# Kernel tuning notes

Measured on AMD Instinct MI355X. Metric: run time of the kernel, lower is better.

Reference implementation:

```python
import jax, jax.numpy as jnp
import numpy as np

INPUT_DIM = 64
AUG_DIM = 64
STATE = INPUT_DIM + AUG_DIM  # 128
HIDDEN = 1024
T = 32
B, S = 64, 64


def setup_inputs() -> dict:
    key = jax.random.key(0)
    ks = jax.random.split(key, 12)

    def lin(kw, kb, out_d, in_d):
        scale = 1.0 / np.sqrt(in_d)
        W = jax.random.uniform(kw, (out_d, in_d), jnp.float32, -scale, scale)
        b = jax.random.uniform(kb, (out_d,), jnp.float32, -scale, scale)
        return W, b

    y0 = jax.random.normal(ks[0], (B, S, INPUT_DIM), jnp.float32)
    t = jnp.linspace(0.0, 1.0, T, dtype=jnp.float32)
    W_aug, b_aug = lin(ks[1], ks[2], AUG_DIM, INPUT_DIM)
    W0, b0 = lin(ks[3], ks[4], HIDDEN, STATE)
    W1, b1 = lin(ks[5], ks[6], HIDDEN, HIDDEN)
    W2, b2 = lin(ks[7], ks[8], HIDDEN, HIDDEN)
    W3, b3 = lin(ks[9], ks[10], STATE, HIDDEN)
    return {"y0": y0, "t": t, "W_aug": W_aug, "b_aug": b_aug,
            "W0": W0, "b0": b0, "W1": W1, "b1": b1,
            "W2": W2, "b2": b2, "W3": W3, "b3": b3}


def reference(y0, t, W_aug, b_aug, W0, b0, W1, b1, W2, b2, W3, b3):
    # augment: y0 [B,S,Din] -> [B,S,Din+Daug]
    y_aug = jnp.einsum('bsd,ad->bsa', y0, W_aug) + b_aug
    y = jnp.concatenate([y0, y_aug], axis=-1)  # [B,S,STATE]

    dt = t[1] - t[0]

    def mlp(z):
        h = jnp.tanh(jnp.einsum('bsd,hd->bsh', z, W0) + b0)
        h = jnp.tanh(jnp.einsum('bsh,gh->bsg', h, W1) + b1)
        h = jnp.tanh(jnp.einsum('bsh,gh->bsg', h, W2) + b2)
        return jnp.einsum('bsh,dh->bsd', h, W3) + b3

    def step(y_cur, _):
        y_next = y_cur + mlp(y_cur) * dt
        return y_next, None

    # forward only uses the final state: out[:, -1, :, :input_dim]
    y_final, _ = jax.lax.scan(step, y, None, length=T - 1)
    return y_final[..., :INPUT_DIM]
```

## Files before the change

### kernel.cpp

```cpp
#include <hip/hip_runtime.h>

typedef _Float16 h8 __attribute__((ext_vector_type(8)));
typedef float f32x4 __attribute__((ext_vector_type(4)));
typedef int  i4 __attribute__((ext_vector_type(4)));

#define NTHREADS 1024
#define ROWS 16
#define NBLK 256

#define SMEM_BYTES 163840

#define GLOAD16(gp, lp) __builtin_amdgcn_global_load_lds( \
    (const __attribute__((address_space(1))) void*)(gp),  \
    (__attribute__((address_space(3))) void*)(lp), 16, 0, 0)

__device__ __forceinline__ float fast_tanh(float x) {
    float e = __expf(2.0f * x);
    return 1.0f - 2.0f / (e + 1.0f);
}

__device__ __forceinline__ void lightbar() {
    asm volatile("s_waitcnt lgkmcnt(0)" ::: "memory");
    __builtin_amdgcn_sched_barrier(0);
    __builtin_amdgcn_s_barrier();
    __builtin_amdgcn_sched_barrier(0);
}

template<int K>
__global__ void __launch_bounds__(256) pack_kernel(const float* __restrict__ src,
                                                   _Float16* __restrict__ dst, int nfrag) {
    constexpr int NK = K / 32;
    int idx = blockIdx.x * 256 + threadIdx.x;
    if (idx >= nfrag) return;
    int lane = idx & 63;
    int ct   = (idx >> 6) & 3;
    int kk   = (idx >> 8) % NK;
    int w    = idx / (256 * NK);
    int col  = w * 64 + ct * 16 + (lane & 15);
    int kb   = kk * 32 + (lane >> 4) * 8;
    const float* s = src + (size_t)col * K + kb;
    f32x4 v0 = *(const f32x4*)s;
    f32x4 v1 = *(const f32x4*)(s + 4);
    h8 h;
    h[0]=(_Float16)v0[0]; h[1]=(_Float16)v0[1]; h[2]=(_Float16)v0[2]; h[3]=(_Float16)v0[3];
    h[4]=(_Float16)v1[0]; h[5]=(_Float16)v1[1]; h[6]=(_Float16)v1[2]; h[7]=(_Float16)v1[3];
    *(h8*)(dst + (size_t)idx * 8) = h;
}

__global__ void __launch_bounds__(256) pack8_kernel(const float* __restrict__ src,
                                                    char* __restrict__ dst, int nfrag) {
    int idx = blockIdx.x * 256 + threadIdx.x;
    if (idx >= nfrag) return;
    int lane = idx & 63;
    int ct   = (idx >> 6) & 3;
    int kk   = (idx >> 8) & 15;
    int w    = idx >> 12;
    int col  = w * 64 + ct * 16 + (lane & 15);
    int kb   = kk * 64 + (lane >> 4) * 16;
    const float* s = src + (size_t)col * 1024 + kb;
    union { char q[16]; i4 v; } u;
#pragma unroll
    for (int j = 0; j < 16; ++j)
        u.q[j] = (char)__float2int_rn(s[j] * 4064.0f);
    *(i4*)(dst + (size_t)idx * 16) = u.v;
}

__global__ void __launch_bounds__(256) pack3q_kernel(const float* __restrict__ src,
                                                     char* __restrict__ dst, int nfrag) {
    int idx = blockIdx.x * 256 + threadIdx.x;
    if (idx >= nfrag) return;
    int lane = idx & 63;
    int kk   = (idx >> 6) & 15;
    int cg   = idx >> 10;
    int col  = cg * 16 + (lane & 15);
    int kb   = kk * 64 + (lane >> 4) * 16;
    const float* s = src + (size_t)col * 1024 + kb;
    union { char q[16]; i4 v; } u;
#pragma unroll
    for (int j = 0; j < 16; ++j)
        u.q[j] = (char)__float2int_rn(s[j] * 4064.0f);
    *(i4*)(dst + (size_t)idx * 16) = u.v;
}

__device__ __forceinline__ void mlp0(const char* __restrict__ src, char* __restrict__ dst,
                                     const _Float16* __restrict__ Wp, f32x4 bv,
                                     int w, int l15, int lhi, int lane)
{
    constexpr int NK = 4;
    const int colbase = w * 64;
    const _Float16* wb = Wp + (size_t)w * NK * 2048 + lane * 8;

    f32x4 acc[4];
#pragma unroll
    for (int ct = 0; ct < 4; ++ct) {
        f32x4 a; a[0] = bv[ct]; a[1] = bv[ct]; a[2] = bv[ct]; a[3] = bv[ct];
        acc[ct] = a;
    }

    h8 bE[4], bO[4], aE, aO;
    auto loadB = [&](h8* b, int kk) {
#pragma unroll
        for (int ct = 0; ct < 4; ++ct)
            b[ct] = *(const h8*)(wb + (size_t)kk * 2048 + ct * 512);
    };
    auto loadA = [&](h8& a, int kk) {
        int byte = (l15 * 256 + kk * 64 + lhi * 16) ^ ((l15 & 7) << 4);
        a = *(const h8*)(src + byte);
    };
    auto mfma4 = [&](h8& a, h8* b) {
        __builtin_amdgcn_s_setprio(1);
#pragma unroll
        for (int ct = 0; ct < 4; ++ct)
            acc[ct] = __builtin_amdgcn_mfma_f32_16x16x32_f16(a, b[ct], acc[ct], 0, 0, 0);
        __builtin_amdgcn_s_setprio(0);
    };

    loadB(bE, 0); loadA(aE, 0);
    loadB(bO, 1); loadA(aO, 1);
    mfma4(aE, bE);
    loadB(bE, 2); loadA(aE, 2);
    mfma4(aO, bO);
    loadB(bO, 3); loadA(aO, 3);
    mfma4(aE, bE);
    mfma4(aO, bO);

#pragma unroll
    for (int ct = 0; ct < 4; ++ct)
#pragma unroll
        for (int j = 0; j < 4; ++j) {
            int row = lhi * 4 + j;
            int gc = colbase + ct * 16 + l15;
            int q = __float2int_rn(fast_tanh(acc[ct][j]) * 127.0f);
            int byte = (row * 1024 + gc) ^ ((row & 7) << 4);
            *(char*)(dst + byte) = (char)q;
        }
}

__device__ __forceinline__ void stage2(const char* wbl, char* ringW)
{
#pragma unroll
    for (int c = 0; c < 2; ++c) {
        const char* g = wbl + (size_t)c * 4096;
        char* l = ringW + c * 4096;
#pragma unroll
        for (int ct = 0; ct < 4; ++ct)
            GLOAD16(g + ct * 1024, l + ct * 1024);
    }
}

__device__ __forceinline__ void mlp8c(const char* __restrict__ src, char* __restrict__ dst,
                                      const char* wbl, char* ringW, const char* ringR,
                                      f32x4 bv, int w, int l15, int lhi,
                                      const char* nextwb)
{
    const int colbase = w * 64;
    i4 acc[4];
#pragma unroll
    for (int ct = 0; ct < 4; ++ct) { i4 z; z[0]=0; z[1]=0; z[2]=0; z[3]=0; acc[ct] = z; }

    i4 B0, B1, B2, B3, A;
    auto readSlot = [&](int kk) {
        const char* sl = ringR + (kk & 1) * 4096;
        B0 = *(const i4*)(sl);
        B1 = *(const i4*)(sl + 1024);
        B2 = *(const i4*)(sl + 2048);
        B3 = *(const i4*)(sl + 3072);
        int byte = (l15 * 1024 + kk * 64 + lhi * 16) ^ ((l15 & 7) << 4);
        A = *(const i4*)(src + byte);
    };
    auto mfma4 = [&]() {
        __builtin_amdgcn_s_setprio(1);
        acc[0] = __builtin_amdgcn_mfma_i32_16x16x64_i8(A, B0, acc[0], 0, 0, 0);
        acc[1] = __builtin_amdgcn_mfma_i32_16x16x64_i8(A, B1, acc[1], 0, 0, 0);
        acc[2] = __builtin_amdgcn_mfma_i32_16x16x64_i8(A, B2, acc[2], 0, 0, 0);
        acc[3] = __builtin_amdgcn_mfma_i32_16x16x64_i8(A, B3, acc[3], 0, 0, 0);
        __builtin_amdgcn_s_setprio(0);
    };

#pragma unroll 1
    for (int kk = 0; kk < 15; ++kk) {
        asm volatile("s_waitcnt vmcnt(4)" ::: "memory");
        __builtin_amdgcn_sched_barrier(0);
        readSlot(kk);
        asm volatile("s_waitcnt lgkmcnt(0)" ::: "memory");
        __builtin_amdgcn_sched_barrier(0);
        if (kk < 14) {
            const char* g = wbl + (size_t)(kk + 2) * 4096;
            char* l = ringW + (kk & 1) * 4096;
#pragma unroll
            for (int ct = 0; ct < 4; ++ct)
                GLOAD16(g + ct * 1024, l + ct * 1024);
        }
        __builtin_amdgcn_sched_barrier(0);
        mfma4();
    }
    asm volatile("s_waitcnt vmcnt(0)" ::: "memory");
    __builtin_amdgcn_sched_barrier(0);
    readSlot(15);
    asm volatile("s_waitcnt lgkmcnt(0)" ::: "memory");
    __builtin_amdgcn_sched_barrier(0);
    stage2(nextwb, ringW);
    __builtin_amdgcn_sched_barrier(0);
    mfma4();

    const float DEQ = 1.0f / 516128.0f;
#pragma unroll
    for (int ct = 0; ct < 4; ++ct) {
        int gc = colbase + ct * 16 + l15;
#pragma unroll
        for (int j = 0; j < 4; ++j) {
            int row = lhi * 4 + j;
            float v = fast_tanh((float)acc[ct][j] * DEQ + bv[ct]);
            int q = __float2int_rn(v * 127.0f);
            int byte = (row * 1024 + gc) ^ ((row & 7) << 4);
            *(char*)(dst + byte) = (char)q;
        }
    }
}

__global__ void
__attribute__((amdgpu_flat_work_group_size(NTHREADS, NTHREADS)))
node_kernel(const float* __restrict__ y0,
            const float* __restrict__ tarr,
            const float* __restrict__ W_aug,
            const float* __restrict__ b_aug,
            const float* __restrict__ b0,
            const float* __restrict__ b1,
            const float* __restrict__ b2,
            const float* __restrict__ b3,
            const _Float16* __restrict__ W0p,
            const char* __restrict__ W1q,
            const char* __restrict__ W2q,
            const char* __restrict__ W3q,
            float* __restrict__ out)
{
    __shared__ __align__(16) char smem[SMEM_BYTES];
    char* buf8A = smem;
    char* buf8B = smem + 16384;
    char* Yh    = smem + 16384;
    i4*   red   = (i4*)(smem + 24576);
    float* Yf   = (float*)smem;
    char* ring  = smem + 32768;

    const int tid  = threadIdx.x;
    const int lane = tid & 63;
    const int w    = tid >> 6;
    const int l15  = lane & 15;
    const int lhi  = lane >> 4;
    const int row0 = blockIdx.x * ROWS;

    const float dtv = tarr[1] - tarr[0];

    if (tid < 256) {
        int idx = tid * 4;
        int r = idx >> 6;
        int c = idx & 63;
        f32x4 v = *(const f32x4*)(y0 + (size_t)(row0 + r) * 64 + c);
        *(f32x4*)(Yf + r * 128 + c) = v;
    }
    __syncthreads();

    {
        int r = tid >> 6;
        int a0 = tid & 63;
        float acc = b_aug[a0];
        for (int d = 0; d < 64; ++d)
            acc += Yf[r * 128 + d] * W_aug[a0 * 64 + d];
        __syncthreads();
        Yf[r * 128 + 64 + a0] = acc;
    }
    __syncthreads();

    const int g = w * 16 + l15;
    f32x4 yreg;
    if (w < 8) {
#pragma unroll
        for (int j = 0; j < 4; ++j)
            yreg[j] = Yf[(lhi * 4 + j) * 128 + g];
    }
    h8 yh0;
    int yh0_byte;
    if (tid < 256) {
        int r = tid >> 4;
        int c = (tid & 15) * 8;
        const float* p = Yf + r * 128 + c;
#pragma unroll
        for (int j = 0; j < 8; ++j) yh0[j] = (_Float16)p[j];
        yh0_byte = ((r * 128 + c) * 2) ^ ((r & 7) << 4);
    }
    __syncthreads();
    if (tid < 256) *(h8*)(Yh + yh0_byte) = yh0;
    __syncthreads();

    const char* wb1 = W1q + (size_t)w * 65536 + lane * 16;
    const char* wb2 = W2q + (size_t)w * 65536 + lane * 16;
    char* ringW = ring + w * 8192;
    const char* ringR = ringW + lane * 16;

    f32x4 b0v, b1v, b2v;
#pragma unroll
    for (int ct = 0; ct < 4; ++ct) {
        b0v[ct] = b0[w * 64 + ct * 16 + l15];
        b1v[ct] = b1[w * 64 + ct * 16 + l15];
        b2v[ct] = b2[w * 64 + ct * 16 + l15];
    }
    const int cg  = w & 7;
    const int kk0 = (w >> 3) * 8;
    const char* wb3 = W3q + (size_t)cg * 16384 + lane * 16;
    const float b3v = (w < 8) ? b3[g] : 0.0f;
    const float DEQ3 = 1.0f / 516128.0f;

    stage2(wb1, ringW);

    for (int s = 0; s < 31; ++s) {
        mlp0(Yh, buf8A, W0p, b0v, w, l15, lhi, lane);
        lightbar();

        mlp8c(buf8A, buf8B, wb1, ringW, ringR, b1v, w, l15, lhi, wb2);
        lightbar();

        mlp8c(buf8B, buf8A, wb2, ringW, ringR, b2v, w, l15, lhi, wb1);
        lightbar();

        {
            i4 acc3; acc3[0]=0; acc3[1]=0; acc3[2]=0; acc3[3]=0;
            i4 c3E, c3O, x3E, x3O;
            auto loadB3 = [&](i4& b, int kk) {
                b = *(const i4*)(wb3 + (size_t)kk * 1024);
            };
            auto loadA3 = [&](i4& a, int kk) {
                int byte = (l15 * 1024 + kk * 64 + lhi * 16) ^ ((l15 & 7) << 4);
                a = *(const i4*)(buf8A + byte);
            };
            loadB3(c3E, kk0 + 0); loadA3(x3E, kk0 + 0);
#pragma unroll
            for (int q = 0; q < 3; ++q) {
                loadB3(c3O, kk0 + 2 * q + 1); loadA3(x3O, kk0 + 2 * q + 1);
                acc3 = __builtin_amdgcn_mfma_i32_16x16x64_i8(x3E, c3E, acc3, 0, 0, 0);
                loadB3(c3E, kk0 + 2 * q + 2); loadA3(x3E, kk0 + 2 * q + 2);
                acc3 = __builtin_amdgcn_mfma_i32_16x16x64_i8(x3O, c3O, acc3, 0, 0, 0);
            }
            loadB3(c3O, kk0 + 7); loadA3(x3O, kk0 + 7);
            acc3 = __builtin_amdgcn_mfma_i32_16x16x64_i8(x3E, c3E, acc3, 0, 0, 0);
            acc3 = __builtin_amdgcn_mfma_i32_16x16x64_i8(x3O, c3O, acc3, 0, 0, 0);

            if (w >= 8)
                red[cg * 64 + lane] = acc3;
            lightbar();
            if (w < 8) {
                i4 part = red[w * 64 + lane];
#pragma unroll
                for (int j = 0; j < 4; ++j) {
                    int row = lhi * 4 + j;
                    float dy = (float)(acc3[j] + part[j]) * DEQ3 + b3v;
                    float nv = yreg[j] + dtv * dy;
                    yreg[j] = nv;
                    int byte = ((row * 128 + g) * 2) ^ ((row & 7) << 4);
                    *(_Float16*)(Yh + byte) = (_Float16)nv;
                }
            }
        }
        lightbar();
    }

    asm volatile("s_waitcnt vmcnt(0)" ::: "memory");

    if (w < 4) {
#pragma unroll
        for (int j = 0; j < 4; ++j) {
            int row = lhi * 4 + j;
            out[(size_t)(row0 + row) * 64 + g] = yreg[j];
        }
    }
}

extern "C" void kernel_launch(void* const* d_in, const int* in_sizes, int n_in,
                              void* d_out, int out_size, void* d_ws, size_t ws_size,
                              hipStream_t stream)
{
    const float* y0    = (const float*)d_in[0];
    const float* tarr  = (const float*)d_in[1];
    const float* W_aug = (const float*)d_in[2];
    const float* b_aug = (const float*)d_in[3];
    const float* W0    = (const float*)d_in[4];
    const float* b0    = (const float*)d_in[5];
    const float* W1    = (const float*)d_in[6];
    const float* b1    = (const float*)d_in[7];
    const float* W2    = (const float*)d_in[8];
    const float* b2    = (const float*)d_in[9];
    const float* W3    = (const float*)d_in[10];
    const float* b3    = (const float*)d_in[11];

    _Float16* W0p = (_Float16*)d_ws;
    char* W1q = (char*)d_ws + 262144;
    char* W2q = (char*)d_ws + 1310720;
    char* W3q = (char*)d_ws + 2359296;

    pack_kernel<128><<<16384 / 256, 256, 0, stream>>>(W0, W0p, 16384);
    pack8_kernel<<<65536 / 256, 256, 0, stream>>>(W1, W1q, 65536);
    pack8_kernel<<<65536 / 256, 256, 0, stream>>>(W2, W2q, 65536);
    pack3q_kernel<<<8192 / 256, 256, 0, stream>>>(W3, W3q, 8192);

    node_kernel<<<NBLK, NTHREADS, 0, stream>>>(y0, tarr, W_aug, b_aug,
                                               b0, b1, b2, b3,
                                               W0p, W1q, W2q, W3q,
                                               (float*)d_out);
}
```

Baseline: 1.241 ms.

## Deepen weight staging ring to four 2KB slots with prefetch distance three

Restructures the weight streaming in the int8 hidden layers from a 2-slot ring of 4KB chunks (prefetch distance 2, with a tail that drains the queue) into a 4-slot ring of 2KB chunks with prefetch distance 3. The loop is fully unrolled, and each half-chunk feeds two MFMAs. The next layer's weights are prefetched continuously, so there is no vmcnt(0) drain at the end. The goal is to keep more global-to-LDS loads in flight and hide memory latency better. The cost is more waitcnt/barrier points per K step, a fully unrolled 32-iteration loop that enlarges the code, and a vmcnt(4) threshold that must stay consistent with the deeper ring.

```diff
diff --git a/kernel.cpp b/kernel.cpp
--- a/kernel.cpp
+++ b/kernel.cpp
@@ -136,72 +136,62 @@
         }
 }
 
-__device__ __forceinline__ void stage2(const char* wbl, char* ringW)
-{
-#pragma unroll
-    for (int c = 0; c < 2; ++c) {
-        const char* g = wbl + (size_t)c * 4096;
-        char* l = ringW + c * 4096;
-#pragma unroll
-        for (int ct = 0; ct < 4; ++ct)
-            GLOAD16(g + ct * 1024, l + ct * 1024);
-    }
+__device__ __forceinline__ void stage_chunk(const char* g, char* l) {
+    GLOAD16(g, l);
+    GLOAD16(g + 1024, l + 1024);
+}
+
+__device__ __forceinline__ void stage3(const char* wbl, char* ringW) {
+#pragma unroll
+    for (int c = 0; c < 3; ++c)
+        stage_chunk(wbl + (size_t)c * 2048, ringW + (c & 3) * 2048);
 }
 
 __device__ __forceinline__ void mlp8c(const char* __restrict__ src, char* __restrict__ dst,
-                                      const char* wbl, char* ringW, const char* ringR,
-                                      f32x4 bv, int w, int l15, int lhi,
-                                      const char* nextwb)
+                                      const char* wbl, const char* nextwb,
+                                      char* ringW, const char* ringR,
+                                      f32x4 bv, int w, int l15, int lhi)
 {
     const int colbase = w * 64;
     i4 acc[4];
 #pragma unroll
     for (int ct = 0; ct < 4; ++ct) { i4 z; z[0]=0; z[1]=0; z[2]=0; z[3]=0; acc[ct] = z; }
 
-    i4 B0, B1, B2, B3, A;
-    auto readSlot = [&](int kk) {
-        const char* sl = ringR + (kk & 1) * 4096;
-        B0 = *(const i4*)(sl);
-        B1 = *(const i4*)(sl + 1024);
-        B2 = *(const i4*)(sl + 2048);
-        B3 = *(const i4*)(sl + 3072);
-        int byte = (l15 * 1024 + kk * 64 + lhi * 16) ^ ((l15 & 7) << 4);
-        A = *(const i4*)(src + byte);
-    };
-    auto mfma4 = [&]() {
-        __builtin_amdgcn_s_setprio(1);
-        acc[0] = __builtin_amdgcn_mfma_i32_16x16x64_i8(A, B0, acc[0], 0, 0, 0);
-        acc[1] = __builtin_amdgcn_mfma_i32_16x16x64_i8(A, B1, acc[1], 0, 0, 0);
-        acc[2] = __builtin_amdgcn_mfma_i32_16x16x64_i8(A, B2, acc[2], 0, 0, 0);
-        acc[3] = __builtin_amdgcn_mfma_i32_16x16x64_i8(A, B3, acc[3], 0, 0, 0);
-        __builtin_amdgcn_s_setprio(0);
-    };
-
-#pragma unroll 1
-    for (int kk = 0; kk < 15; ++kk) {
+    i4 A{}, B0, B1;
+
+#pragma unroll
+    for (int c = 0; c < 32; ++c) {
         asm volatile("s_waitcnt vmcnt(4)" ::: "memory");
         __builtin_amdgcn_sched_barrier(0);
-        readSlot(kk);
+        {
+            const char* g = (c + 3 < 32) ? (wbl + (size_t)(c + 3) * 2048)
+                                         : (nextwb + (size_t)(c + 3 - 32) * 2048);
+            char* l = ringW + ((c + 3) & 3) * 2048;
+            stage_chunk(g, l);
+        }
+        __builtin_amdgcn_sched_barrier(0);
+        {
+            const char* sl = ringR + (c & 3) * 2048;
+            B0 = *(const i4*)(sl);
+            B1 = *(const i4*)(sl + 1024);
+        }
+        if ((c & 1) == 0) {
+            int kk = c >> 1;
+            int byte = (l15 * 1024 + kk * 64 + lhi * 16) ^ ((l15 & 7) << 4);
+            A = *(const i4*)(src + byte);
+        }
         asm volatile("s_waitcnt lgkmcnt(0)" ::: "memory");
         __builtin_amdgcn_sched_barrier(0);
-        if (kk < 14) {
-            const char* g = wbl + (size_t)(kk + 2) * 4096;
-            char* l = ringW + (kk & 1) * 4096;
-#pragma unroll
-            for (int ct = 0; ct < 4; ++ct)
-                GLOAD16(g + ct * 1024, l + ct * 1024);
-        }
-        __builtin_amdgcn_sched_barrier(0);
-        mfma4();
-    }
-    asm volatile("s_waitcnt vmcnt(0)" ::: "memory");
-    __builtin_amdgcn_sched_barrier(0);
-    readSlot(15);
-    asm volatile("s_waitcnt lgkmcnt(0)" ::: "memory");
-    __builtin_amdgcn_sched_barrier(0);
-    stage2(nextwb, ringW);
-    __builtin_amdgcn_sched_barrier(0);
-    mfma4();
+        __builtin_amdgcn_s_setprio(1);
+        if ((c & 1) == 0) {
+            acc[0] = __builtin_amdgcn_mfma_i32_16x16x64_i8(A, B0, acc[0], 0, 0, 0);
+            acc[1] = __builtin_amdgcn_mfma_i32_16x16x64_i8(A, B1, acc[1], 0, 0, 0);
+        } else {
+            acc[2] = __builtin_amdgcn_mfma_i32_16x16x64_i8(A, B0, acc[2], 0, 0, 0);
+            acc[3] = __builtin_amdgcn_mfma_i32_16x16x64_i8(A, B1, acc[3], 0, 0, 0);
+        }
+        __builtin_amdgcn_s_setprio(0);
+    }
 
     const float DEQ = 1.0f / 516128.0f;
 #pragma unroll
@@ -310,16 +300,16 @@
     const float b3v = (w < 8) ? b3[g] : 0.0f;
     const float DEQ3 = 1.0f / 516128.0f;
 
-    stage2(wb1, ringW);
+    stage3(wb1, ringW);
 
     for (int s = 0; s < 31; ++s) {
         mlp0(Yh, buf8A, W0p, b0v, w, l15, lhi, lane);
         lightbar();
 
-        mlp8c(buf8A, buf8B, wb1, ringW, ringR, b1v, w, l15, lhi, wb2);
+        mlp8c(buf8A, buf8B, wb1, wb2, ringW, ringR, b1v, w, l15, lhi);
         lightbar();
 
-        mlp8c(buf8B, buf8A, wb2, ringW, ringR, b2v, w, l15, lhi, wb1);
+        mlp8c(buf8B, buf8A, wb2, wb1, ringW, ringR, b2v, w, l15, lhi);
         lightbar();
 
         {
```

Result: slower. 3.107 ms (+150.3%).
